# Performance work log

Measured on AMD Instinct MI355X. Metric: run time of the kernel, lower is better.

Reference implementation:

```python
import jax, jax.numpy as jnp
import numpy as np

B, N, DIM = 2, 2048, 512
HEADS, DIM_HEAD = 8, 64
INNER = HEADS * DIM_HEAD
SCALE = DIM_HEAD ** -0.5
ALPHA = 32.0 ** 2  # stable_softmax alpha


def setup_inputs() -> dict:
    key = jax.random.key(0)
    k1, k2, k3, k4 = jax.random.split(key, 4)
    x = jax.random.normal(k1, (B, N, DIM), dtype=jnp.float32)
    mask = jnp.ones((B, N), dtype=bool)
    # nn.Linear(dim, inner*3, bias=False) -> stored transposed for x @ W
    w_qkv = jax.random.normal(k2, (DIM, INNER * 3), dtype=jnp.float32) * (DIM ** -0.5)
    w_out = jax.random.normal(k3, (INNER, DIM), dtype=jnp.float32) * (INNER ** -0.5)
    b_out = jax.random.normal(k4, (DIM,), dtype=jnp.float32) * 0.01
    return {"x": x, "mask": mask, "w_qkv": w_qkv, "w_out": w_out, "b_out": b_out}


def stable_softmax(t, alpha=ALPHA):
    t = t / alpha
    t = t - jnp.max(t, axis=-1, keepdims=True)
    return jax.nn.softmax(t * alpha, axis=-1)


def reference(x, mask, w_qkv, w_out, b_out):
    b, n, _ = x.shape
    qkv = x @ w_qkv  # [b, n, 3*inner]
    q, k, v = jnp.split(qkv, 3, axis=-1)
    # 'b n (h d) -> b h n d'
    split_heads = lambda t: t.reshape(b, n, HEADS, DIM_HEAD).transpose(0, 2, 1, 3)
    q, k, v = split_heads(q), split_heads(k), split_heads(v)
    q = q * SCALE
    dots = jnp.einsum('bhid,bhjd->bhij', q, k)  # [b, h, n, n]
    mask_value = -jnp.finfo(dots.dtype).max
    # key padding mask: 'b j -> b 1 1 j'
    dots = jnp.where(mask[:, None, None, :], dots, mask_value)
    # causal mask: triu with offset j - i + 1 == 1 here
    causal = jnp.triu(jnp.ones((n, n), dtype=bool), k=1)
    dots = jnp.where(causal, mask_value, dots)
    attn = stable_softmax(dots)
    out = jnp.einsum('bhij,bhjd->bhid', attn, v)
    out = out.transpose(0, 2, 1, 3).reshape(b, n, INNER)  # 'b h n d -> b n (h d)'
    return out @ w_out + b_out
```

## Files before the change

### kernel.cpp

```cpp
#include <hip/hip_runtime.h>
#include <hip/hip_bf16.h>
#include <stdint.h>

#define B_ 2
#define N_ 2048
#define DIM_ 512
#define HEADS_ 8
#define DHEAD_ 64
#define INNER_ 512

typedef float f32x4 __attribute__((ext_vector_type(4)));
typedef float f32x16 __attribute__((ext_vector_type(16)));
typedef __bf16 bf16x8 __attribute__((ext_vector_type(8)));
typedef unsigned short us8 __attribute__((ext_vector_type(8)));
typedef unsigned short us4 __attribute__((ext_vector_type(4)));
typedef unsigned int u32x4 __attribute__((ext_vector_type(4)));

static __device__ __forceinline__ unsigned short f2bf(float f) {
    union { float f; unsigned int u; } v; v.f = f;
    unsigned int r = v.u + 0x7fffu + ((v.u >> 16) & 1u);
    return (unsigned short)(r >> 16);
}

static __device__ __forceinline__ float exp2_fast(float x) {
    return __builtin_amdgcn_exp2f(x);
}

static __device__ __forceinline__ unsigned cvtpk(float lo, float hi) {
    unsigned r;
    asm("v_cvt_pk_bf16_f32 %0, %1, %2" : "=v"(r) : "v"(lo), "v"(hi));
    return r;
}

static __device__ __forceinline__ f32x4 mfma16(bf16x8 a, bf16x8 b, f32x4 c) {
    return __builtin_amdgcn_mfma_f32_16x16x32_bf16(a, b, c, 0, 0, 0);
}
static __device__ __forceinline__ f32x16 mfma32(bf16x8 a, bf16x8 b, f32x16 c) {
    return __builtin_amdgcn_mfma_f32_32x32x16_bf16(a, b, c, 0, 0, 0);
}

static __device__ __forceinline__ size_t qk_off(int bh, int n, int d) {
    int T = n >> 5, r = n & 31, c = d >> 4, s = d & 15;
    return ((((size_t)bh * 64 + T) * 4 + c) << 9) + (size_t)(((s >> 3) * 32 + r) * 8 + (s & 7));
}
static __device__ __forceinline__ size_t vt_off(int bh, int d, int n) {
    int tt = n >> 5, kv = n & 31;
    int mi = (kv >> 4) & 1, g = (kv >> 2) & 1;
    int jj = (kv & 3) + 4 * ((kv >> 3) & 1);
    int dblk = d >> 5;
    int lane = (d & 31) + 32 * g;
    return ((((size_t)bh * 64 + tt) * 2 + dblk) * 2 + mi) * 512 + (size_t)(lane * 8 + jj);
}

__global__ __launch_bounds__(256) void k_transpose_w(const float* __restrict__ wqkv,
                                                     const float* __restrict__ wout,
                                                     unsigned short* __restrict__ oqkv,
                                                     unsigned short* __restrict__ oout,
                                                     float qscale) {
    __shared__ float tile[32][33];
    const int tx = threadIdx.x & 31, ty = threadIdx.x >> 5;
    const bool isQ = blockIdx.y < 48;
    const float* in = isQ ? wqkv : wout;
    unsigned short* out = isQ ? oqkv : oout;
    const int N = isQ ? 1536 : 512;
    const int scale_cols = isQ ? 512 : 0;
    const int K = 512;
    const int k0 = blockIdx.x * 32, n0 = (isQ ? blockIdx.y : blockIdx.y - 48) * 32;
#pragma unroll
    for (int j = 0; j < 4; j++)
        tile[ty + 8 * j][tx] = in[(size_t)(k0 + ty + 8 * j) * N + n0 + tx];
    __syncthreads();
#pragma unroll
    for (int j = 0; j < 4; j++) {
        int n = n0 + ty + 8 * j;
        float v = tile[tx][ty + 8 * j];
        if (n < scale_cols) v *= qscale;
        out[(size_t)n * K + k0 + tx] = f2bf(v);
    }
}

template <int MODE>
__global__ __launch_bounds__(256) void k_gemm(const void* __restrict__ Av,
                                              const unsigned short* __restrict__ Bt,
                                              int K, int Ncols,
                                              float* __restrict__ Cf,
                                              const float* __restrict__ bias,
                                              unsigned short* __restrict__ Qb,
                                              unsigned short* __restrict__ Kb,
                                              unsigned short* __restrict__ Vt) {
    __shared__ unsigned short As[128 * 72];
    __shared__ unsigned short Bs[128 * 72];
    const int t = threadIdx.x;
    const int lane = t & 63;
    const int w = t >> 6;
    const int wy = w >> 1, wx = w & 1;
    const int lo = lane & 15, hi = lane >> 4;

    const int ncolb = Ncols >> 7;
    const int bid = blockIdx.x;
    const int wg = (bid & 7) * ((int)gridDim.x >> 3) + (bid >> 3);
    const int row0 = (wg / ncolb) * 128, col0 = (wg % ncolb) * 128;

    f32x4 acc[4][4];
#pragma unroll
    for (int m = 0; m < 4; m++)
#pragma unroll
        for (int n = 0; n < 4; n++) acc[m][n] = 0.f;

    for (int k0 = 0; k0 < K; k0 += 64) {
#pragma unroll
        for (int i = 0; i < 4; i++) {
            int chunk = t + i * 256;
            int r = chunk >> 3;
            int c = (chunk & 7) << 3;
            if (MODE == 0) {
                const float* Af = (const float*)Av;
                float4 v0 = *(const float4*)&Af[(size_t)(row0 + r) * K + k0 + c];
                float4 v1 = *(const float4*)&Af[(size_t)(row0 + r) * K + k0 + c + 4];
                us8 o;
                o[0] = f2bf(v0.x); o[1] = f2bf(v0.y); o[2] = f2bf(v0.z); o[3] = f2bf(v0.w);
                o[4] = f2bf(v1.x); o[5] = f2bf(v1.y); o[6] = f2bf(v1.z); o[7] = f2bf(v1.w);
                *(us8*)&As[r * 72 + c] = o;
            } else {
                const unsigned short* Ab = (const unsigned short*)Av;
                *(us8*)&As[r * 72 + c] = *(const us8*)&Ab[(size_t)(row0 + r) * K + k0 + c];
            }
            *(us8*)&Bs[r * 72 + c] = *(const us8*)&Bt[(size_t)(col0 + r) * K + k0 + c];
        }
        __syncthreads();
#pragma unroll
        for (int ks = 0; ks < 2; ks++) {
            bf16x8 af[4], bfr[4];
#pragma unroll
            for (int m = 0; m < 4; m++)
                af[m] = *(const bf16x8*)&As[(wy * 64 + m * 16 + lo) * 72 + ks * 32 + hi * 8];
#pragma unroll
            for (int n = 0; n < 4; n++)
                bfr[n] = *(const bf16x8*)&Bs[(wx * 64 + n * 16 + lo) * 72 + ks * 32 + hi * 8];
#pragma unroll
            for (int m = 0; m < 4; m++)
#pragma unroll
                for (int n = 0; n < 4; n++)
                    acc[m][n] = mfma16(af[m], bfr[n], acc[m][n]);
        }
        __syncthreads();
    }

#pragma unroll
    for (int m = 0; m < 4; m++) {
#pragma unroll
        for (int n = 0; n < 4; n++) {
#pragma unroll
            for (int r = 0; r < 4; r++) {
                int row = row0 + wy * 64 + m * 16 + hi * 4 + r;
                int col = col0 + wx * 64 + n * 16 + lo;
                float v = acc[m][n][r];
                if (MODE == 0) {
                    unsigned short bv = f2bf(v);
                    int b = row >> 11, nn = row & 2047;
                    int sec = col >> 9, cc = col & 511;
                    int h = cc >> 6, d = cc & 63;
                    int bh = b * HEADS_ + h;
                    if (sec == 0)      Qb[qk_off(bh, nn, d)] = bv;
                    else if (sec == 1) Kb[qk_off(bh, nn, d)] = bv;
                    else               Vt[vt_off(bh, d, nn)] = bv;
                } else {
                    Cf[(size_t)row * Ncols + col] = v + bias[col];
                }
            }
        }
    }
}


static __device__ __forceinline__ void pack_P(const f32x16& sT, bf16x8& P0, bf16x8& P1) {
    u32x4 pw0, pw1;
    pw0[0] = cvtpk(sT[0], sT[1]);   pw0[1] = cvtpk(sT[2], sT[3]);
    pw0[2] = cvtpk(sT[4], sT[5]);   pw0[3] = cvtpk(sT[6], sT[7]);
    pw1[0] = cvtpk(sT[8], sT[9]);   pw1[1] = cvtpk(sT[10], sT[11]);
    pw1[2] = cvtpk(sT[12], sT[13]); pw1[3] = cvtpk(sT[14], sT[15]);
    P0 = __builtin_bit_cast(bf16x8, pw0);
    P1 = __builtin_bit_cast(bf16x8, pw1);
}

static __device__ __forceinline__ void do_tile(
    const unsigned short* kbase, const unsigned short* vbase, int tt,
    bool diag, int qg, int half,
    const bf16x8 (&qf)[4],
    float& m_, float& l_, f32x16& o0, f32x16& o1) {
    const unsigned short* kp = kbase + (size_t)tt * 2048;
    bf16x8 kf0 = *(const bf16x8*)(kp);
    bf16x8 kf1 = *(const bf16x8*)(kp + 512);
    bf16x8 kf2 = *(const bf16x8*)(kp + 1024);
    bf16x8 kf3 = *(const bf16x8*)(kp + 1536);
    const unsigned short* vp = vbase + (size_t)tt * 2048;
    bf16x8 vf00 = *(const bf16x8*)(vp);
    bf16x8 vf01 = *(const bf16x8*)(vp + 512);
    bf16x8 vf10 = *(const bf16x8*)(vp + 1024);
    bf16x8 vf11 = *(const bf16x8*)(vp + 1536);

    f32x16 sT = 0.f;
    sT = mfma32(kf0, qf[0], sT);
    sT = mfma32(kf1, qf[1], sT);
    sT = mfma32(kf2, qf[2], sT);
    sT = mfma32(kf3, qf[3], sT);

    if (diag) {
        const int kv0 = tt * 32;
#pragma unroll
        for (int r = 0; r < 16; r++) {
            int kv = kv0 + (r & 3) + 8 * (r >> 2) + 4 * half;
            if (kv > qg) sT[r] = -1e30f;
        }
    }

    float a0 = fmaxf(sT[0], sT[1]),  a1 = fmaxf(sT[2], sT[3]);
    float a2 = fmaxf(sT[4], sT[5]),  a3 = fmaxf(sT[6], sT[7]);
    float a4 = fmaxf(sT[8], sT[9]),  a5 = fmaxf(sT[10], sT[11]);
    float a6 = fmaxf(sT[12], sT[13]), a7 = fmaxf(sT[14], sT[15]);
    float mx = fmaxf(fmaxf(fmaxf(a0, a1), fmaxf(a2, a3)),
                     fmaxf(fmaxf(a4, a5), fmaxf(a6, a7)));

    bool need = __any(mx > m_ + 11.f);
    if (need) {
        mx = fmaxf(mx, __shfl_xor(mx, 32, 64));
        float mn = fmaxf(m_, mx);
        float al = exp2_fast(m_ - mn);
        m_ = mn;
        l_ *= al;
#pragma unroll
        for (int r = 0; r < 16; r++) { o0[r] *= al; o1[r] *= al; }
    }

#pragma unroll
    for (int r = 0; r < 16; r++) sT[r] = exp2_fast(sT[r] - m_);
    float b0 = sT[0] + sT[1],   b1 = sT[2] + sT[3];
    float b2 = sT[4] + sT[5],   b3 = sT[6] + sT[7];
    float b4 = sT[8] + sT[9],   b5 = sT[10] + sT[11];
    float b6 = sT[12] + sT[13], b7 = sT[14] + sT[15];
    l_ += ((b0 + b1) + (b2 + b3)) + ((b4 + b5) + (b6 + b7));

    bf16x8 P0, P1;
    pack_P(sT, P0, P1);
    o0 = mfma32(vf00, P0, o0);
    o0 = mfma32(vf01, P1, o0);
    o1 = mfma32(vf10, P0, o1);
    o1 = mfma32(vf11, P1, o1);
}

static __device__ __forceinline__ void publish_merge2(
    float (*Osh)[32 * 33], float (*Msh)[32], float (*Lsh)[64],
    int t, int w, int q31, int half, int bh, int q0,
    float m_, float l_, const f32x16& o0, const f32x16& o1,
    unsigned short* __restrict__ attb) {
    const int b = bh >> 3, h = bh & 7;
    float* ow = Osh[w];
#pragma unroll
    for (int r = 0; r < 16; r++) {
        int d = (r & 3) + 8 * (r >> 2) + 4 * half;
        ow[q31 * 33 + d] = o0[r];
    }
    Lsh[w][half * 32 + q31] = l_;
    if (half == 0) Msh[w][q31] = m_;
    __syncthreads();

    float mg = -1e30f, inv = 0.f;
    const int mq = (t >> 3) & 31, d0 = (t & 7) * 4;
    if (t < 256) {
#pragma unroll
        for (int w2 = 0; w2 < 8; w2++) mg = fmaxf(mg, Msh[w2][mq]);
        float Lg = 0.f;
        float acc[4] = {0.f, 0.f, 0.f, 0.f};
#pragma unroll
        for (int w2 = 0; w2 < 8; w2++) {
            float f = exp2_fast(Msh[w2][mq] - mg);
            Lg += (Lsh[w2][mq] + Lsh[w2][32 + mq]) * f;
#pragma unroll
            for (int i = 0; i < 4; i++) acc[i] += Osh[w2][mq * 33 + d0 + i] * f;
        }
        inv = 1.f / Lg;
        us4 ov;
#pragma unroll
        for (int i = 0; i < 4; i++) ov[i] = f2bf(acc[i] * inv);
        *(us4*)&attb[((size_t)b * N_ + q0 + mq) * INNER_ + h * DHEAD_ + d0] = ov;
    }
    __syncthreads();

#pragma unroll
    for (int r = 0; r < 16; r++) {
        int d = (r & 3) + 8 * (r >> 2) + 4 * half;
        ow[q31 * 33 + d] = o1[r];
    }
    __syncthreads();
    if (t < 256) {
        float acc[4] = {0.f, 0.f, 0.f, 0.f};
#pragma unroll
        for (int w2 = 0; w2 < 8; w2++) {
            float f = exp2_fast(Msh[w2][mq] - mg);
#pragma unroll
            for (int i = 0; i < 4; i++) acc[i] += Osh[w2][mq * 33 + d0 + i] * f;
        }
        us4 ov;
#pragma unroll
        for (int i = 0; i < 4; i++) ov[i] = f2bf(acc[i] * inv);
        *(us4*)&attb[((size_t)b * N_ + q0 + mq) * INNER_ + h * DHEAD_ + 32 + d0] = ov;
    }
    __syncthreads();
}

__global__ __launch_bounds__(512, 4) void k_attn(const unsigned short* __restrict__ Qb,
                                                 const unsigned short* __restrict__ Kb,
                                                 const unsigned short* __restrict__ Vt,
                                                 unsigned short* __restrict__ attb) {
    __shared__ float Osh[8][32 * 33];
    __shared__ float Msh[8][32];
    __shared__ float Lsh[8][64];
    const int t = threadIdx.x, lane = t & 63, w = t >> 6;
    const int q31 = lane & 31, half = lane >> 5;

    int wg = (blockIdx.x & 7) * 64 + (blockIdx.x >> 3);
    const int bh = wg >> 5;
    const int pa = wg & 31;
    const int pb = 63 - pa;

    const unsigned short* kbase = Kb + (size_t)bh * 131072 + lane * 8;
    const unsigned short* vbase = Vt + (size_t)bh * 131072 + lane * 8;
    const unsigned short* qbh   = Qb + (size_t)bh * 131072 + lane * 8;

#pragma unroll
    for (int s = 0; s < 2; s++) {
        const int p = s ? pb : pa;
        const int q0 = p * 32, qg = q0 + q31;
        const unsigned short* qp = qbh + (size_t)p * 2048;
        bf16x8 qf[4];
        qf[0] = *(const bf16x8*)(qp);
        qf[1] = *(const bf16x8*)(qp + 512);
        qf[2] = *(const bf16x8*)(qp + 1024);
        qf[3] = *(const bf16x8*)(qp + 1536);
        float m_ = -1e30f, l_ = 0.f;
        f32x16 o0 = 0.f, o1 = 0.f;
        for (int tt = w; tt <= p; tt += 8)
            do_tile(kbase, vbase, tt, tt == p, qg, half, qf, m_, l_, o0, o1);
        publish_merge2(Osh, Msh, Lsh, t, w, q31, half, bh, q0, m_, l_, o0, o1, attb);
    }
}

extern "C" void kernel_launch(void* const* d_in, const int* in_sizes, int n_in,
                              void* d_out, int out_size, void* d_ws, size_t ws_size,
                              hipStream_t stream) {
    const float* x     = (const float*)d_in[0];
    const float* w_qkv = (const float*)d_in[2];
    const float* w_out = (const float*)d_in[3];
    const float* b_out = (const float*)d_in[4];
    float* out = (float*)d_out;

    char* ws = (char*)d_ws;
    size_t off = 0;
    auto alloc = [&](size_t bytes) {
        void* p = ws + off;
        off += (bytes + 255) & ~(size_t)255;
        return p;
    };
    unsigned short* wqkvt = (unsigned short*)alloc((size_t)1536 * 512 * 2);
    unsigned short* woutt = (unsigned short*)alloc((size_t)512 * 512 * 2);
    unsigned short* Qb    = (unsigned short*)alloc((size_t)16 * 2048 * 64 * 2);
    unsigned short* Kb    = (unsigned short*)alloc((size_t)16 * 2048 * 64 * 2);
    unsigned short* Vt    = (unsigned short*)alloc((size_t)16 * 2048 * 64 * 2);
    unsigned short* attb  = (unsigned short*)alloc((size_t)4096 * 512 * 2);

    const float QSCALE = 0.125f * 1.44269504088896340736f;
    k_transpose_w<<<dim3(16, 64), 256, 0, stream>>>(w_qkv, w_out, wqkvt, woutt, QSCALE);
    k_gemm<0><<<384, 256, 0, stream>>>(x, wqkvt, 512, 1536, nullptr, nullptr, Qb, Kb, Vt);
    k_attn<<<512, 512, 0, stream>>>(Qb, Kb, Vt, attb);
    k_gemm<1><<<128, 256, 0, stream>>>(attb, woutt, 512, 512, out, b_out, nullptr, nullptr, nullptr);
}
```

Baseline: 61.27 us.

## Share K/V tile loads between paired query blocks in attention loop

The two causal-balanced query blocks handled by each workgroup used to be processed one after the other, each loading K/V tiles separately. They are now processed in a single loop where each K/V tile is loaded once and used for both query blocks while the tile index is within the shorter block's range. This halves K/V global loads for the overlapping tiles but keeps two sets of accumulators live, so register pressure rises. To absorb that, launch bounds are relaxed from 4 to 2 waves per SIMD, which may lower occupancy.

```diff
diff --git a/kernel.cpp b/kernel.cpp
--- a/kernel.cpp
+++ b/kernel.cpp
@@ -173,6 +173,26 @@
 }
 
 
+struct KV {
+    bf16x8 k0, k1, k2, k3;
+    bf16x8 v0, v1, v2, v3;
+};
+
+static __device__ __forceinline__ void load_kv(const unsigned short* kbase,
+                                               const unsigned short* vbase,
+                                               int tt, KV& f) {
+    const unsigned short* kp = kbase + (size_t)tt * 2048;
+    f.k0 = *(const bf16x8*)(kp);
+    f.k1 = *(const bf16x8*)(kp + 512);
+    f.k2 = *(const bf16x8*)(kp + 1024);
+    f.k3 = *(const bf16x8*)(kp + 1536);
+    const unsigned short* vp = vbase + (size_t)tt * 2048;
+    f.v0 = *(const bf16x8*)(vp);
+    f.v1 = *(const bf16x8*)(vp + 512);
+    f.v2 = *(const bf16x8*)(vp + 1024);
+    f.v3 = *(const bf16x8*)(vp + 1536);
+}
+
 static __device__ __forceinline__ void pack_P(const f32x16& sT, bf16x8& P0, bf16x8& P1) {
     u32x4 pw0, pw1;
     pw0[0] = cvtpk(sT[0], sT[1]);   pw0[1] = cvtpk(sT[2], sT[3]);
@@ -183,27 +203,15 @@
     P1 = __builtin_bit_cast(bf16x8, pw1);
 }
 
-static __device__ __forceinline__ void do_tile(
-    const unsigned short* kbase, const unsigned short* vbase, int tt,
-    bool diag, int qg, int half,
+static __device__ __forceinline__ void compute_tile(
+    const KV& f, int tt, bool diag, int qg, int half,
     const bf16x8 (&qf)[4],
     float& m_, float& l_, f32x16& o0, f32x16& o1) {
-    const unsigned short* kp = kbase + (size_t)tt * 2048;
-    bf16x8 kf0 = *(const bf16x8*)(kp);
-    bf16x8 kf1 = *(const bf16x8*)(kp + 512);
-    bf16x8 kf2 = *(const bf16x8*)(kp + 1024);
-    bf16x8 kf3 = *(const bf16x8*)(kp + 1536);
-    const unsigned short* vp = vbase + (size_t)tt * 2048;
-    bf16x8 vf00 = *(const bf16x8*)(vp);
-    bf16x8 vf01 = *(const bf16x8*)(vp + 512);
-    bf16x8 vf10 = *(const bf16x8*)(vp + 1024);
-    bf16x8 vf11 = *(const bf16x8*)(vp + 1536);
-
     f32x16 sT = 0.f;
-    sT = mfma32(kf0, qf[0], sT);
-    sT = mfma32(kf1, qf[1], sT);
-    sT = mfma32(kf2, qf[2], sT);
-    sT = mfma32(kf3, qf[3], sT);
+    sT = mfma32(f.k0, qf[0], sT);
+    sT = mfma32(f.k1, qf[1], sT);
+    sT = mfma32(f.k2, qf[2], sT);
+    sT = mfma32(f.k3, qf[3], sT);
 
     if (diag) {
         const int kv0 = tt * 32;
@@ -242,10 +250,10 @@
 
     bf16x8 P0, P1;
     pack_P(sT, P0, P1);
-    o0 = mfma32(vf00, P0, o0);
-    o0 = mfma32(vf01, P1, o0);
-    o1 = mfma32(vf10, P0, o1);
-    o1 = mfma32(vf11, P1, o1);
+    o0 = mfma32(f.v0, P0, o0);
+    o0 = mfma32(f.v1, P1, o0);
+    o1 = mfma32(f.v2, P0, o1);
+    o1 = mfma32(f.v3, P1, o1);
 }
 
 static __device__ __forceinline__ void publish_merge2(
@@ -308,7 +316,7 @@
     __syncthreads();
 }
 
-__global__ __launch_bounds__(512, 4) void k_attn(const unsigned short* __restrict__ Qb,
+__global__ __launch_bounds__(512, 2) void k_attn(const unsigned short* __restrict__ Qb,
                                                  const unsigned short* __restrict__ Kb,
                                                  const unsigned short* __restrict__ Vt,
                                                  unsigned short* __restrict__ attb) {
@@ -327,22 +335,32 @@
     const unsigned short* vbase = Vt + (size_t)bh * 131072 + lane * 8;
     const unsigned short* qbh   = Qb + (size_t)bh * 131072 + lane * 8;
 
-#pragma unroll
-    for (int s = 0; s < 2; s++) {
-        const int p = s ? pb : pa;
-        const int q0 = p * 32, qg = q0 + q31;
-        const unsigned short* qp = qbh + (size_t)p * 2048;
-        bf16x8 qf[4];
-        qf[0] = *(const bf16x8*)(qp);
-        qf[1] = *(const bf16x8*)(qp + 512);
-        qf[2] = *(const bf16x8*)(qp + 1024);
-        qf[3] = *(const bf16x8*)(qp + 1536);
-        float m_ = -1e30f, l_ = 0.f;
-        f32x16 o0 = 0.f, o1 = 0.f;
-        for (int tt = w; tt <= p; tt += 8)
-            do_tile(kbase, vbase, tt, tt == p, qg, half, qf, m_, l_, o0, o1);
-        publish_merge2(Osh, Msh, Lsh, t, w, q31, half, bh, q0, m_, l_, o0, o1, attb);
-    }
+    const int qgA = pa * 32 + q31, qgB = pb * 32 + q31;
+    const unsigned short* qpA = qbh + (size_t)pa * 2048;
+    const unsigned short* qpB = qbh + (size_t)pb * 2048;
+    bf16x8 qfA[4], qfB[4];
+    qfA[0] = *(const bf16x8*)(qpA);
+    qfA[1] = *(const bf16x8*)(qpA + 512);
+    qfA[2] = *(const bf16x8*)(qpA + 1024);
+    qfA[3] = *(const bf16x8*)(qpA + 1536);
+    qfB[0] = *(const bf16x8*)(qpB);
+    qfB[1] = *(const bf16x8*)(qpB + 512);
+    qfB[2] = *(const bf16x8*)(qpB + 1024);
+    qfB[3] = *(const bf16x8*)(qpB + 1536);
+
+    float mA = -1e30f, lA = 0.f, mB = -1e30f, lB = 0.f;
+    f32x16 oA0 = 0.f, oA1 = 0.f, oB0 = 0.f, oB1 = 0.f;
+
+    KV f;
+    for (int tt = w; tt <= pb; tt += 8) {
+        load_kv(kbase, vbase, tt, f);
+        if (tt <= pa)
+            compute_tile(f, tt, tt == pa, qgA, half, qfA, mA, lA, oA0, oA1);
+        compute_tile(f, tt, tt == pb, qgB, half, qfB, mB, lB, oB0, oB1);
+    }
+
+    publish_merge2(Osh, Msh, Lsh, t, w, q31, half, bh, pa * 32, mA, lA, oA0, oA1, attb);
+    publish_merge2(Osh, Msh, Lsh, t, w, q31, half, bh, pb * 32, mB, lB, oB0, oB1, attb);
 }
 
 extern "C" void kernel_launch(void* const* d_in, const int* in_sizes, int n_in,
```

Result: slower. 63.52 us (+3.7%).

## Split attention KV range across two blocks with a separate merge kernel

Applied to the files above, without the earlier changes.

Doubles the attention grid by splitting each query-pair's work into two blocks. One block does the short tile pa plus the KV tiles 32 and up for pb. The other does KV tiles 0 to 31 for pb. Partial O, M and L values are written to workspace in fp32, and a new k_merge kernel combines them into bf16 output. This is meant to improve occupancy and balance across the 256 CUs, at the cost of an extra launch and extra global traffic for the fp32 partials.

```diff
diff --git a/kernel.cpp b/kernel.cpp
--- a/kernel.cpp
+++ b/kernel.cpp
@@ -308,30 +308,119 @@
     __syncthreads();
 }
 
+static __device__ __forceinline__ void publish_partial(
+    float (*Osh)[32 * 33], float (*Msh)[32], float (*Lsh)[64],
+    int t, int w, int q31, int half,
+    float m_, float l_, const f32x16& o0, const f32x16& o1,
+    float* __restrict__ Op, float* __restrict__ Mp, float* __restrict__ Lp) {
+    float* ow = Osh[w];
+#pragma unroll
+    for (int r = 0; r < 16; r++) {
+        int d = (r & 3) + 8 * (r >> 2) + 4 * half;
+        ow[q31 * 33 + d] = o0[r];
+    }
+    Lsh[w][half * 32 + q31] = l_;
+    if (half == 0) Msh[w][q31] = m_;
+    __syncthreads();
+
+    float mg = -1e30f;
+    const int mq = (t >> 3) & 31, d0 = (t & 7) * 4;
+    if (t < 256) {
+#pragma unroll
+        for (int w2 = 0; w2 < 8; w2++) mg = fmaxf(mg, Msh[w2][mq]);
+        float Lg = 0.f;
+        f32x4 acc = 0.f;
+#pragma unroll
+        for (int w2 = 0; w2 < 8; w2++) {
+            float f = exp2_fast(Msh[w2][mq] - mg);
+            Lg += (Lsh[w2][mq] + Lsh[w2][32 + mq]) * f;
+#pragma unroll
+            for (int i = 0; i < 4; i++) acc[i] += Osh[w2][mq * 33 + d0 + i] * f;
+        }
+        *(f32x4*)&Op[mq * 64 + d0] = acc;
+        if ((t & 7) == 0) { Mp[mq] = mg; Lp[mq] = Lg; }
+    }
+    __syncthreads();
+
+#pragma unroll
+    for (int r = 0; r < 16; r++) {
+        int d = (r & 3) + 8 * (r >> 2) + 4 * half;
+        ow[q31 * 33 + d] = o1[r];
+    }
+    __syncthreads();
+    if (t < 256) {
+        f32x4 acc = 0.f;
+#pragma unroll
+        for (int w2 = 0; w2 < 8; w2++) {
+            float f = exp2_fast(Msh[w2][mq] - mg);
+#pragma unroll
+            for (int i = 0; i < 4; i++) acc[i] += Osh[w2][mq * 33 + d0 + i] * f;
+        }
+        *(f32x4*)&Op[mq * 64 + 32 + d0] = acc;
+    }
+    __syncthreads();
+}
+
 __global__ __launch_bounds__(512, 4) void k_attn(const unsigned short* __restrict__ Qb,
                                                  const unsigned short* __restrict__ Kb,
                                                  const unsigned short* __restrict__ Vt,
-                                                 unsigned short* __restrict__ attb) {
+                                                 unsigned short* __restrict__ attb,
+                                                 float* __restrict__ Op,
+                                                 float* __restrict__ Mp,
+                                                 float* __restrict__ Lp) {
     __shared__ float Osh[8][32 * 33];
     __shared__ float Msh[8][32];
     __shared__ float Lsh[8][64];
     const int t = threadIdx.x, lane = t & 63, w = t >> 6;
     const int q31 = lane & 31, half = lane >> 5;
 
-    int wg = (blockIdx.x & 7) * 64 + (blockIdx.x >> 3);
-    const int bh = wg >> 5;
-    const int pa = wg & 31;
-    const int pb = 63 - pa;
+    int wg = (blockIdx.x & 7) * 128 + (blockIdx.x >> 3);
+    const int bh = wg >> 6;
+    const int pp = (wg >> 1) & 31;
+    const int kvh = wg & 1;
+    const int pa = pp, pb = 63 - pp;
 
     const unsigned short* kbase = Kb + (size_t)bh * 131072 + lane * 8;
     const unsigned short* vbase = Vt + (size_t)bh * 131072 + lane * 8;
     const unsigned short* qbh   = Qb + (size_t)bh * 131072 + lane * 8;
 
-#pragma unroll
-    for (int s = 0; s < 2; s++) {
-        const int p = s ? pb : pa;
-        const int q0 = p * 32, qg = q0 + q31;
-        const unsigned short* qp = qbh + (size_t)p * 2048;
+    const size_t pidx = (size_t)(bh * 32 + pp) * 2 + kvh;
+    float* Opb = Op + pidx * 2048;
+    float* Mpb = Mp + pidx * 32;
+    float* Lpb = Lp + pidx * 32;
+
+    if (kvh == 1) {
+        {
+            const int q0 = pa * 32, qg = q0 + q31;
+            const unsigned short* qp = qbh + (size_t)pa * 2048;
+            bf16x8 qf[4];
+            qf[0] = *(const bf16x8*)(qp);
+            qf[1] = *(const bf16x8*)(qp + 512);
+            qf[2] = *(const bf16x8*)(qp + 1024);
+            qf[3] = *(const bf16x8*)(qp + 1536);
+            float m_ = -1e30f, l_ = 0.f;
+            f32x16 o0 = 0.f, o1 = 0.f;
+            for (int tt = w; tt <= pa; tt += 8)
+                do_tile(kbase, vbase, tt, tt == pa, qg, half, qf, m_, l_, o0, o1);
+            publish_merge2(Osh, Msh, Lsh, t, w, q31, half, bh, q0, m_, l_, o0, o1, attb);
+        }
+        {
+            const int q0 = pb * 32, qg = q0 + q31;
+            const unsigned short* qp = qbh + (size_t)pb * 2048;
+            bf16x8 qf[4];
+            qf[0] = *(const bf16x8*)(qp);
+            qf[1] = *(const bf16x8*)(qp + 512);
+            qf[2] = *(const bf16x8*)(qp + 1024);
+            qf[3] = *(const bf16x8*)(qp + 1536);
+            float m_ = -1e30f, l_ = 0.f;
+            f32x16 o0 = 0.f, o1 = 0.f;
+            for (int tt = 32 + w; tt <= pb; tt += 8)
+                do_tile(kbase, vbase, tt, tt == pb, qg, half, qf, m_, l_, o0, o1);
+            publish_partial(Osh, Msh, Lsh, t, w, q31, half, m_, l_, o0, o1, Opb, Mpb, Lpb);
+        }
+    } else {
+        const int q0 = pb * 32, qg = q0 + q31;
+        const unsigned short* qp = qbh + (size_t)pb * 2048;
         bf16x8 qf[4];
         qf[0] = *(const bf16x8*)(qp);
         qf[1] = *(const bf16x8*)(qp + 512);
@@ -339,10 +428,36 @@
         qf[3] = *(const bf16x8*)(qp + 1536);
         float m_ = -1e30f, l_ = 0.f;
         f32x16 o0 = 0.f, o1 = 0.f;
-        for (int tt = w; tt <= p; tt += 8)
-            do_tile(kbase, vbase, tt, tt == p, qg, half, qf, m_, l_, o0, o1);
-        publish_merge2(Osh, Msh, Lsh, t, w, q31, half, bh, q0, m_, l_, o0, o1, attb);
-    }
+        for (int tt = w; tt < 32; tt += 8)
+            do_tile(kbase, vbase, tt, false, qg, half, qf, m_, l_, o0, o1);
+        publish_partial(Osh, Msh, Lsh, t, w, q31, half, m_, l_, o0, o1, Opb, Mpb, Lpb);
+    }
+}
+
+__global__ __launch_bounds__(256) void k_merge(const float* __restrict__ Op,
+                                               const float* __restrict__ Mp,
+                                               const float* __restrict__ Lp,
+                                               unsigned short* __restrict__ attb) {
+    const int bid = blockIdx.x;
+    const int bh = bid >> 5, pp = bid & 31;
+    const int pb = 63 - pp;
+    const int t = threadIdx.x;
+    const int row = t >> 3, d0 = (t & 7) * 8;
+    const size_t i0 = (size_t)(bh * 32 + pp) * 2;
+    const size_t i1 = i0 + 1;
+    float M0 = Mp[i0 * 32 + row], L0 = Lp[i0 * 32 + row];
+    float M1 = Mp[i1 * 32 + row], L1 = Lp[i1 * 32 + row];
+    float ms = fmaxf(M0, M1);
+    float f0 = exp2_fast(M0 - ms), f1 = exp2_fast(M1 - ms);
+    float inv = 1.f / (L0 * f0 + L1 * f1);
+    const float* O0 = Op + i0 * 2048 + row * 64 + d0;
+    const float* O1 = Op + i1 * 2048 + row * 64 + d0;
+    us8 ov;
+#pragma unroll
+    for (int i = 0; i < 8; i++)
+        ov[i] = f2bf((O0[i] * f0 + O1[i] * f1) * inv);
+    const int b = bh >> 3, h = bh & 7;
+    *(us8*)&attb[((size_t)b * N_ + pb * 32 + row) * INNER_ + h * DHEAD_ + d0] = ov;
 }
 
 extern "C" void kernel_launch(void* const* d_in, const int* in_sizes, int n_in,
@@ -367,10 +482,14 @@
     unsigned short* Kb    = (unsigned short*)alloc((size_t)16 * 2048 * 64 * 2);
     unsigned short* Vt    = (unsigned short*)alloc((size_t)16 * 2048 * 64 * 2);
     unsigned short* attb  = (unsigned short*)alloc((size_t)4096 * 512 * 2);
+    float* Op = (float*)alloc((size_t)16 * 32 * 2 * 2048 * 4);
+    float* Mp = (float*)alloc((size_t)16 * 32 * 2 * 32 * 4);
+    float* Lp = (float*)alloc((size_t)16 * 32 * 2 * 32 * 4);
 
     const float QSCALE = 0.125f * 1.44269504088896340736f;
     k_transpose_w<<<dim3(16, 64), 256, 0, stream>>>(w_qkv, w_out, wqkvt, woutt, QSCALE);
     k_gemm<0><<<384, 256, 0, stream>>>(x, wqkvt, 512, 1536, nullptr, nullptr, Qb, Kb, Vt);
-    k_attn<<<512, 512, 0, stream>>>(Qb, Kb, Vt, attb);
+    k_attn<<<1024, 512, 0, stream>>>(Qb, Kb, Vt, attb, Op, Mp, Lp);
+    k_merge<<<512, 256, 0, stream>>>(Op, Mp, Lp, attb);
     k_gemm<1><<<128, 256, 0, stream>>>(attb, woutt, 512, 512, out, b_out, nullptr, nullptr, nullptr);
 }
```

Result: slower. 70.03 us (+14.3%).
